# Performance work log

Hardware: AMD Instinct MI355X
Metric: run time of the kernel (lower is better)

Reference implementation:

```python
import jax, jax.numpy as jnp
import numpy as np

IN_DIM = 128
D_MODEL = 2 * IN_DIM        # 256, Mamba d_model
D_INNER = 2 * D_MODEL       # 512, expand=2
D_STATE = 16
D_CONV = 4
DT_RANK = (D_MODEL + 15) // 16  # 16
B = 4
C = 1024                    # original channel dim -> Mamba sequence length
EPS = 1e-5


def rmsnorm(x, w):
    return x * jax.lax.rsqrt(jnp.mean(x * x, axis=-1, keepdims=True) + EPS) * w


def conv1x1(x, w, b):
    # x: (B, Cin, L); 1x1 conv == channel matmul
    return jnp.einsum('oi,bil->bol', w, x) + b[None, :, None]


def mamba(u, in_w, conv_w, conv_b, xproj_w, dt_w, dt_b, A_log, Dp, out_w):
    # u: (B, L, D_MODEL) -- faithful mamba_ssm Mamba block (defaults)
    di, K = conv_w.shape
    n = A_log.shape[1]
    r = dt_w.shape[1]
    xz = u @ in_w.T                              # (B,L,2*di)
    xx, z = jnp.split(xz, 2, axis=-1)
    # depthwise causal conv over L
    xt = jnp.pad(jnp.transpose(xx, (0, 2, 1)), ((0, 0), (0, 0), (K - 1, 0)))
    xc = jax.lax.conv_general_dilated(xt, conv_w[:, None, :], (1,), 'VALID',
                                      feature_group_count=di)
    xx = jax.nn.silu(jnp.transpose(xc + conv_b[None, :, None], (0, 2, 1)))
    dbl = xx @ xproj_w.T                         # (B,L,r+2n)
    dt, Bm, Cm = dbl[..., :r], dbl[..., r:r + n], dbl[..., r + n:]
    dt = jax.nn.softplus(dt @ dt_w.T + dt_b)     # (B,L,di)
    A = -jnp.exp(A_log)                          # (di,n)
    dA = jnp.exp(dt[..., None] * A)              # (B,L,di,n)
    dBx = (dt * xx)[..., None] * Bm[:, :, None, :]

    def step(h, inps):
        dA_t, dBx_t, C_t = inps
        h = dA_t * h + dBx_t
        return h, jnp.einsum('bdn,bn->bd', h, C_t)

    h0 = jnp.zeros((u.shape[0], di, n), u.dtype)
    _, ys = jax.lax.scan(step, h0, (jnp.moveaxis(dA, 1, 0),
                                    jnp.moveaxis(dBx, 1, 0),
                                    jnp.moveaxis(Cm, 1, 0)))
    y = jnp.moveaxis(ys, 0, 1) + xx * Dp
    return (y * jax.nn.silu(z)) @ out_w.T


def postnorm_mamba(u, params, norm_w):
    return rmsnorm(mamba(u, *params), norm_w) + u


def _forward(x, W_in, b_in, W_wp, b_wp, W_fp, b_fp, W_bp, b_bp, W_out, b_out,
             norm_w_top,
             f_in_w, f_conv_w, f_conv_b, f_xproj_w, f_dt_w, f_dt_b, f_A_log, f_D, f_out_w, f_norm_w,
             bk_in_w, bk_conv_w, bk_conv_b, bk_xproj_w, bk_dt_w, bk_dt_b, bk_A_log, bk_D, bk_out_w, bk_norm_w):
    residual = x                                  # (B, C, L)
    xn = rmsnorm(x, norm_w_top)                   # RMSNorm over L
    xt = jnp.transpose(xn, (0, 2, 1))             # (B, L, C); L acts as conv channels
    ssm_in = conv1x1(xt, W_in, b_in)              # (B, 2L, C)
    # forward branch
    fwd = conv1x1(ssm_in, W_fp, b_fp)
    fwd = jnp.transpose(fwd, (0, 2, 1))           # (B, C, 2L): Mamba seq=C
    fwd = postnorm_mamba(fwd, (f_in_w, f_conv_w, f_conv_b, f_xproj_w, f_dt_w,
                               f_dt_b, f_A_log, f_D, f_out_w), f_norm_w)
    fwd = jnp.transpose(fwd, (0, 2, 1))           # (B, 2L, C)
    # backward branch (flip along C)
    bwd = conv1x1(ssm_in[:, :, ::-1], W_bp, b_bp)
    bwd = jnp.transpose(bwd, (0, 2, 1))
    bwd = postnorm_mamba(bwd, (bk_in_w, bk_conv_w, bk_conv_b, bk_xproj_w, bk_dt_w,
                               bk_dt_b, bk_A_log, bk_D, bk_out_w), bk_norm_w)
    bwd = jnp.transpose(bwd, (0, 2, 1))[:, :, ::-1]
    # swish gate
    w = conv1x1(xt, W_wp, b_wp)
    w = w * jax.nn.sigmoid(w)
    out = conv1x1(w * fwd + w * bwd, W_out, b_out)  # (B, L, C)
    return jnp.transpose(out, (0, 2, 1)) + residual  # (B, C, L)


def setup_inputs():
    key = jax.random.key(0)
    ks = iter(jax.random.split(key, 64))
    rn = lambda shape, s=0.02: jax.random.normal(next(ks), shape, jnp.float32) * s
    inp = {"x": jax.random.normal(next(ks), (B, C, IN_DIM), jnp.float32)}
    inp["W_in"] = rn((2 * IN_DIM, IN_DIM));   inp["b_in"] = rn((2 * IN_DIM,), 0.1)
    inp["W_wp"] = rn((2 * IN_DIM, IN_DIM));   inp["b_wp"] = rn((2 * IN_DIM,), 0.1)
    inp["W_fp"] = rn((2 * IN_DIM, 2 * IN_DIM)); inp["b_fp"] = rn((2 * IN_DIM,), 0.1)
    inp["W_bp"] = rn((2 * IN_DIM, 2 * IN_DIM)); inp["b_bp"] = rn((2 * IN_DIM,), 0.1)
    inp["W_out"] = rn((IN_DIM, 2 * IN_DIM));  inp["b_out"] = rn((IN_DIM,), 0.1)
    inp["norm_w_top"] = jnp.ones((IN_DIM,), jnp.float32)
    A_init = jnp.log(jnp.broadcast_to(jnp.arange(1, D_STATE + 1, dtype=jnp.float32),
                                      (D_INNER, D_STATE)))
    for p in ("f", "bk"):
        inp[p + "_in_w"] = rn((2 * D_INNER, D_MODEL))
        inp[p + "_conv_w"] = rn((D_INNER, D_CONV), 0.2)
        inp[p + "_conv_b"] = rn((D_INNER,), 0.1)
        inp[p + "_xproj_w"] = rn((DT_RANK + 2 * D_STATE, D_INNER))
        inp[p + "_dt_w"] = rn((D_INNER, DT_RANK), 0.1)
        inp[p + "_dt_b"] = rn((D_INNER,), 0.5)
        inp[p + "_A_log"] = A_init
        inp[p + "_D"] = jnp.ones((D_INNER,), jnp.float32)
        inp[p + "_out_w"] = rn((D_MODEL, D_INNER))
        inp[p + "_norm_w"] = jnp.ones((D_MODEL,), jnp.float32)
    return inp


def reference(x, W_in, b_in, W_wp, b_wp, W_fp, b_fp, W_bp, b_bp, W_out, b_out,
              norm_w_top,
              f_in_w, f_conv_w, f_conv_b, f_xproj_w, f_dt_w, f_dt_b, f_A_log, f_D, f_out_w, f_norm_w,
              bk_in_w, bk_conv_w, bk_conv_b, bk_xproj_w, bk_dt_w, bk_dt_b, bk_A_log, bk_D, bk_out_w, bk_norm_w):
    return _forward(x, W_in, b_in, W_wp, b_wp, W_fp, b_fp, W_bp, b_bp, W_out, b_out,
                    norm_w_top,
                    f_in_w, f_conv_w, f_conv_b, f_xproj_w, f_dt_w, f_dt_b, f_A_log, f_D, f_out_w, f_norm_w,
                    bk_in_w, bk_conv_w, bk_conv_b, bk_xproj_w, bk_dt_w, bk_dt_b, bk_A_log, bk_D, bk_out_w, bk_norm_w)
```

## Files before the change

### kernel.cpp

```cpp
#include <hip/hip_runtime.h>
#include <math.h>

#define C_LEN 1024
#define NROW 4096
#define NCHUNK 32
#define CHUNK 32

typedef __attribute__((ext_vector_type(8))) short short8;
typedef __attribute__((ext_vector_type(4))) float f32x4;

__device__ __forceinline__ float siluf(float x) { return x / (1.f + __expf(-x)); }

__device__ __forceinline__ unsigned short f2bf(float f) {
    unsigned u = __builtin_bit_cast(unsigned, f);
    unsigned r = (u + 0x7FFFu + ((u >> 16) & 1u)) >> 16;
    return (unsigned short)r;
}
__device__ __forceinline__ float bf2f(unsigned short v) {
    unsigned u = ((unsigned)v) << 16;
    return __builtin_bit_cast(float, u);
}

struct WTab {
    const float* s[11];
    unsigned short* d[11];
    int n[11];
};
__global__ __launch_bounds__(256) void k_prep(WTab t, const float* __restrict__ x,
                                              const float* __restrict__ nw,
                                              unsigned short* __restrict__ xn_bf) {
    int seg = blockIdx.y;
    if (seg < 11) {
        int n = t.n[seg];
        int i = (blockIdx.x * 256 + threadIdx.x) * 4;
        if (i < n) {
            float4 v = *(const float4*)(t.s[seg] + i);
            unsigned short* o = t.d[seg] + i;
            o[0] = f2bf(v.x); o[1] = f2bf(v.y); o[2] = f2bf(v.z); o[3] = f2bf(v.w);
        }
    } else {
        int wave = threadIdx.x >> 6, lane = threadIdx.x & 63;
        #pragma unroll
        for (int it = 0; it < 4; ++it) {
            int row = blockIdx.x * 16 + it * 4 + wave;
            float2 v = ((const float2*)(x + (size_t)row * 128))[lane];
            float ss = v.x * v.x + v.y * v.y;
            #pragma unroll
            for (int off = 32; off; off >>= 1) ss += __shfl_xor(ss, off, 64);
            float rs = rsqrtf(ss * (1.f / 128.f) + 1e-5f);
            float2 wv = ((const float2*)nw)[lane];
            ushort2 o;
            o.x = f2bf(v.x * rs * wv.x);
            o.y = f2bf(v.y * rs * wv.y);
            ((ushort2*)(xn_bf + (size_t)row * 128))[lane] = o;
        }
    }
}

__global__ __launch_bounds__(256) void k_gemm_bf(const unsigned short* __restrict__ A,
                                                 const unsigned short* __restrict__ W,
                                                 const float* __restrict__ bias,
                                                 unsigned short* __restrict__ Cbf,
                                                 int N, int K) {
    __shared__ __align__(16) unsigned short As[64 * 72];
    __shared__ __align__(16) unsigned short Bs[64 * 72];
    int tid = threadIdx.x;
    int m0 = blockIdx.y * 64, n0 = blockIdx.x * 64;
    int w = tid >> 6, lane = tid & 63;
    int q = lane >> 4, ln = lane & 15;
    int srow = tid >> 2;
    int sseg = (tid & 3) * 16;

    const unsigned short* pa = A + (size_t)(m0 + srow) * K + sseg;
    const unsigned short* pw = W + (size_t)(n0 + srow) * K + sseg;

    f32x4 acc[4];
    #pragma unroll
    for (int j = 0; j < 4; ++j) acc[j] = (f32x4)(0.f);

    for (int k0 = 0; k0 < K; k0 += 64) {
        *(short8*)&As[srow * 72 + sseg]     = *(const short8*)pa;
        *(short8*)&As[srow * 72 + sseg + 8] = *(const short8*)(pa + 8);
        *(short8*)&Bs[srow * 72 + sseg]     = *(const short8*)pw;
        *(short8*)&Bs[srow * 72 + sseg + 8] = *(const short8*)(pw + 8);
        pa += 64; pw += 64;
        __syncthreads();
        short8 af0 = *(const short8*)&As[(w * 16 + ln) * 72 + q * 8];
        short8 af1 = *(const short8*)&As[(w * 16 + ln) * 72 + 32 + q * 8];
        #pragma unroll
        for (int j = 0; j < 4; ++j) {
            short8 bf0 = *(const short8*)&Bs[(j * 16 + ln) * 72 + q * 8];
            short8 bf1 = *(const short8*)&Bs[(j * 16 + ln) * 72 + 32 + q * 8];
            acc[j] = __builtin_amdgcn_mfma_f32_16x16x32_bf16(af0, bf0, acc[j], 0, 0, 0);
            acc[j] = __builtin_amdgcn_mfma_f32_16x16x32_bf16(af1, bf1, acc[j], 0, 0, 0);
        }
        __syncthreads();
    }
    #pragma unroll
    for (int j = 0; j < 4; ++j) {
        int nn = n0 + j * 16 + ln;
        float bsv = bias[nn];
        #pragma unroll
        for (int r = 0; r < 4; ++r) {
            int m = m0 + w * 16 + q * 4 + r;
            Cbf[(size_t)m * N + nn] = f2bf(acc[j][r] + bsv);
        }
    }
}

__global__ __launch_bounds__(256) void k_gemm3(
        const unsigned short* __restrict__ xn, const unsigned short* __restrict__ ssm,
        const unsigned short* __restrict__ Wfp, const unsigned short* __restrict__ Wbp,
        const unsigned short* __restrict__ Wwp,
        const float* __restrict__ bfp, const float* __restrict__ bbp,
        const float* __restrict__ bwp,
        unsigned short* __restrict__ uf, unsigned short* __restrict__ ub,
        unsigned short* __restrict__ wbuf) {
    __shared__ __align__(16) unsigned short As[64 * 72];
    __shared__ __align__(16) unsigned short Bs[64 * 72];
    int z = blockIdx.z;
    const unsigned short* A = (z == 2) ? xn : ssm;
    const unsigned short* W = (z == 0) ? Wfp : (z == 1) ? Wbp : Wwp;
    const float* bias = (z == 0) ? bfp : (z == 1) ? bbp : bwp;
    unsigned short* C = (z == 0) ? uf : (z == 1) ? ub : wbuf;
    int K = (z == 2) ? 128 : 256;
    int tid = threadIdx.x;
    int m0 = blockIdx.y * 64, n0 = blockIdx.x * 64;
    int w = tid >> 6, lane = tid & 63;
    int q = lane >> 4, ln = lane & 15;
    int srow = tid >> 2;
    int sseg = (tid & 3) * 16;

    int mLog = m0 + srow;
    int mPhys = (z == 1) ? (mLog ^ (C_LEN - 1)) : mLog;
    const unsigned short* pa = A + (size_t)mPhys * K + sseg;
    const unsigned short* pw = W + (size_t)(n0 + srow) * K + sseg;

    f32x4 acc[4];
    #pragma unroll
    for (int j = 0; j < 4; ++j) acc[j] = (f32x4)(0.f);

    for (int k0 = 0; k0 < K; k0 += 64) {
        *(short8*)&As[srow * 72 + sseg]     = *(const short8*)pa;
        *(short8*)&As[srow * 72 + sseg + 8] = *(const short8*)(pa + 8);
        *(short8*)&Bs[srow * 72 + sseg]     = *(const short8*)pw;
        *(short8*)&Bs[srow * 72 + sseg + 8] = *(const short8*)(pw + 8);
        pa += 64; pw += 64;
        __syncthreads();
        short8 af0 = *(const short8*)&As[(w * 16 + ln) * 72 + q * 8];
        short8 af1 = *(const short8*)&As[(w * 16 + ln) * 72 + 32 + q * 8];
        #pragma unroll
        for (int j = 0; j < 4; ++j) {
            short8 bf0 = *(const short8*)&Bs[(j * 16 + ln) * 72 + q * 8];
            short8 bf1 = *(const short8*)&Bs[(j * 16 + ln) * 72 + 32 + q * 8];
            acc[j] = __builtin_amdgcn_mfma_f32_16x16x32_bf16(af0, bf0, acc[j], 0, 0, 0);
            acc[j] = __builtin_amdgcn_mfma_f32_16x16x32_bf16(af1, bf1, acc[j], 0, 0, 0);
        }
        __syncthreads();
    }
    #pragma unroll
    for (int j = 0; j < 4; ++j) {
        int nn = n0 + j * 16 + ln;
        float bsv = bias[nn];
        #pragma unroll
        for (int r = 0; r < 4; ++r) {
            int m = m0 + w * 16 + q * 4 + r;
            float v = acc[j][r] + bsv;
            if (z == 2) v = siluf(v);
            C[(size_t)m * 256 + nn] = f2bf(v);
        }
    }
}

__global__ __launch_bounds__(256) void k_gemm128(
        const unsigned short* __restrict__ A0, const unsigned short* __restrict__ A1,
        const unsigned short* __restrict__ W0, const unsigned short* __restrict__ W1,
        unsigned short* __restrict__ Cb0, unsigned short* __restrict__ Cb1,
        int N, int K) {
    __shared__ __align__(16) unsigned short As[128 * 72];
    __shared__ __align__(16) unsigned short Bs[64 * 72];
    int p = blockIdx.z;
    const unsigned short* A = p ? A1 : A0;
    const unsigned short* W = p ? W1 : W0;
    unsigned short* Cbf = p ? Cb1 : Cb0;
    int tid = threadIdx.x;
    int m0 = blockIdx.y * 128, n0 = blockIdx.x * 64;
    int w = tid >> 6, lane = tid & 63;
    int q = lane >> 4, ln = lane & 15;

    int arow0 = tid >> 1;
    int aseg0 = (tid & 1) * 32;
    int brow = tid >> 2, bseg = (tid & 3) * 16;
    const unsigned short* pa = A + (size_t)(m0 + arow0) * K + aseg0;
    const unsigned short* pw = W + (size_t)(n0 + brow) * K + bseg;

    f32x4 acc[2][4];
    #pragma unroll
    for (int i = 0; i < 2; ++i)
        #pragma unroll
        for (int j = 0; j < 4; ++j) acc[i][j] = (f32x4)(0.f);

    for (int k0 = 0; k0 < K; k0 += 64) {
        #pragma unroll
        for (int h = 0; h < 4; ++h)
            *(short8*)&As[arow0 * 72 + aseg0 + h * 8] = *(const short8*)(pa + h * 8);
        *(short8*)&Bs[brow * 72 + bseg]     = *(const short8*)pw;
        *(short8*)&Bs[brow * 72 + bseg + 8] = *(const short8*)(pw + 8);
        pa += 64; pw += 64;
        __syncthreads();
        short8 a0[2], a1[2];
        #pragma unroll
        for (int i = 0; i < 2; ++i) {
            int row = w * 32 + i * 16 + ln;
            a0[i] = *(const short8*)&As[row * 72 + q * 8];
            a1[i] = *(const short8*)&As[row * 72 + 32 + q * 8];
        }
        #pragma unroll
        for (int j = 0; j < 4; ++j) {
            short8 bf0 = *(const short8*)&Bs[(j * 16 + ln) * 72 + q * 8];
            short8 bf1 = *(const short8*)&Bs[(j * 16 + ln) * 72 + 32 + q * 8];
            #pragma unroll
            for (int i = 0; i < 2; ++i) {
                acc[i][j] = __builtin_amdgcn_mfma_f32_16x16x32_bf16(a0[i], bf0, acc[i][j], 0, 0, 0);
                acc[i][j] = __builtin_amdgcn_mfma_f32_16x16x32_bf16(a1[i], bf1, acc[i][j], 0, 0, 0);
            }
        }
        __syncthreads();
    }
    #pragma unroll
    for (int i = 0; i < 2; ++i)
        #pragma unroll
        for (int j = 0; j < 4; ++j) {
            int nn = n0 + j * 16 + ln;
            #pragma unroll
            for (int r = 0; r < 4; ++r) {
                int m = m0 + w * 32 + i * 16 + q * 4 + r;
                Cbf[(size_t)m * N + nn] = f2bf(acc[i][j][r]);
            }
        }
}

__global__ __launch_bounds__(256) void k_gemm2f(
        const unsigned short* __restrict__ A0, const unsigned short* __restrict__ A1,
        const unsigned short* __restrict__ W0, const unsigned short* __restrict__ W1,
        float* __restrict__ Cf0, float* __restrict__ Cf1,
        int N, int K) {
    __shared__ __align__(16) unsigned short As[64 * 72];
    __shared__ __align__(16) unsigned short Bs[64 * 72];
    int p = blockIdx.z;
    const unsigned short* A = p ? A1 : A0;
    const unsigned short* W = p ? W1 : W0;
    float* Cf = p ? Cf1 : Cf0;
    int tid = threadIdx.x;
    int m0 = blockIdx.y * 64, n0 = blockIdx.x * 64;
    int w = tid >> 6, lane = tid & 63;
    int q = lane >> 4, ln = lane & 15;
    int srow = tid >> 2;
    int sseg = (tid & 3) * 16;

    const unsigned short* pa = A + (size_t)(m0 + srow) * K + sseg;
    int nIdx = n0 + srow;
    const unsigned short* pw = W + (size_t)nIdx * K + sseg;
    bool nOK = (nIdx < N);

    f32x4 acc[4];
    #pragma unroll
    for (int j = 0; j < 4; ++j) acc[j] = (f32x4)(0.f);

    for (int k0 = 0; k0 < K; k0 += 64) {
        *(short8*)&As[srow * 72 + sseg]     = *(const short8*)pa;
        *(short8*)&As[srow * 72 + sseg + 8] = *(const short8*)(pa + 8);
        short8 b0 = (short8)(0), b1 = (short8)(0);
        if (nOK) { b0 = *(const short8*)pw; b1 = *(const short8*)(pw + 8); }
        *(short8*)&Bs[srow * 72 + sseg] = b0;
        *(short8*)&Bs[srow * 72 + sseg + 8] = b1;
        pa += 64; pw += 64;
        __syncthreads();
        short8 af0 = *(const short8*)&As[(w * 16 + ln) * 72 + q * 8];
        short8 af1 = *(const short8*)&As[(w * 16 + ln) * 72 + 32 + q * 8];
        #pragma unroll
        for (int j = 0; j < 4; ++j) {
            short8 bf0 = *(const short8*)&Bs[(j * 16 + ln) * 72 + q * 8];
            short8 bf1 = *(const short8*)&Bs[(j * 16 + ln) * 72 + 32 + q * 8];
            acc[j] = __builtin_amdgcn_mfma_f32_16x16x32_bf16(af0, bf0, acc[j], 0, 0, 0);
            acc[j] = __builtin_amdgcn_mfma_f32_16x16x32_bf16(af1, bf1, acc[j], 0, 0, 0);
        }
        __syncthreads();
    }
    #pragma unroll
    for (int j = 0; j < 4; ++j) {
        int nn = n0 + j * 16 + ln;
        if (nn < N) {
            #pragma unroll
            for (int r = 0; r < 4; ++r) {
                int m = m0 + w * 16 + q * 4 + r;
                Cf[(size_t)m * N + nn] = acc[j][r];
            }
        }
    }
}

__global__ __launch_bounds__(256) void k_gemm_comb(const unsigned short* __restrict__ wbuf,
                                                   const unsigned short* __restrict__ mof,
                                                   const unsigned short* __restrict__ mob,
                                                   const unsigned short* __restrict__ W,
                                                   const float* __restrict__ bias,
                                                   const float* __restrict__ resid,
                                                   float* __restrict__ Cf,
                                                   int N, int K) {
    __shared__ __align__(16) unsigned short As[64 * 72];
    __shared__ __align__(16) unsigned short Bs[64 * 72];
    int tid = threadIdx.x;
    int m0 = blockIdx.y * 64, n0 = blockIdx.x * 64;
    int w = tid >> 6, lane = tid & 63;
    int q = lane >> 4, ln = lane & 15;
    int srow = tid >> 2;
    int sseg = (tid & 3) * 16;

    int mLog = m0 + srow;
    int mFlip = mLog ^ (C_LEN - 1);
    int nIdx = n0 + srow;
    const unsigned short* pw = W + (size_t)nIdx * K + sseg;
    bool nOK = (nIdx < N);

    f32x4 acc[4];
    #pragma unroll
    for (int j = 0; j < 4; ++j) acc[j] = (f32x4)(0.f);

    for (int k0 = 0; k0 < K; k0 += 64) {
        size_t off  = (size_t)mLog * 256 + k0 + sseg;
        size_t offb = (size_t)mFlip * 256 + k0 + sseg;
        #pragma unroll
        for (int h = 0; h < 2; ++h) {
            short8 aw = *(const short8*)(wbuf + off + h * 8);
            short8 af = *(const short8*)(mof + off + h * 8);
            short8 ab = *(const short8*)(mob + offb + h * 8);
            short8 av;
            #pragma unroll
            for (int j = 0; j < 8; ++j)
                av[j] = (short)f2bf(bf2f((unsigned short)aw[j]) *
                                    (bf2f((unsigned short)af[j]) + bf2f((unsigned short)ab[j])));
            *(short8*)&As[srow * 72 + sseg + h * 8] = av;
        }
        short8 b0 = (short8)(0), b1 = (short8)(0);
        if (nOK) { b0 = *(const short8*)pw; b1 = *(const short8*)(pw + 8); }
        *(short8*)&Bs[srow * 72 + sseg] = b0;
        *(short8*)&Bs[srow * 72 + sseg + 8] = b1;
        pw += 64;
        __syncthreads();
        short8 af0 = *(const short8*)&As[(w * 16 + ln) * 72 + q * 8];
        short8 af1 = *(const short8*)&As[(w * 16 + ln) * 72 + 32 + q * 8];
        #pragma unroll
        for (int j = 0; j < 4; ++j) {
            short8 bf0 = *(const short8*)&Bs[(j * 16 + ln) * 72 + q * 8];
            short8 bf1 = *(const short8*)&Bs[(j * 16 + ln) * 72 + 32 + q * 8];
            acc[j] = __builtin_amdgcn_mfma_f32_16x16x32_bf16(af0, bf0, acc[j], 0, 0, 0);
            acc[j] = __builtin_amdgcn_mfma_f32_16x16x32_bf16(af1, bf1, acc[j], 0, 0, 0);
        }
        __syncthreads();
    }
    #pragma unroll
    for (int j = 0; j < 4; ++j) {
        int nn = n0 + j * 16 + ln;
        if (nn < N) {
            float bsv = bias[nn];
            #pragma unroll
            for (int r = 0; r < 4; ++r) {
                int m = m0 + w * 16 + q * 4 + r;
                Cf[(size_t)m * N + nn] = acc[j][r] + bsv + resid[(size_t)m * N + nn];
            }
        }
    }
}

__global__ __launch_bounds__(256) void k_conv(const unsigned short* __restrict__ xz0,
                                              const unsigned short* __restrict__ xz1,
                                              const float* __restrict__ cw0,
                                              const float* __restrict__ cw1,
                                              const float* __restrict__ cb0,
                                              const float* __restrict__ cb1,
                                              unsigned short* __restrict__ xc0,
                                              unsigned short* __restrict__ xc1) {
    int pz = blockIdx.z;
    const unsigned short* xz = pz ? xz1 : xz0;
    const float* cw = pz ? cw1 : cw0;
    const float* cb = pz ? cb1 : cb0;
    unsigned short* xconv_bf = pz ? xc1 : xc0;
    int d = blockIdx.x * 256 + threadIdx.x;
    int by = blockIdx.y;
    int b = by >> 6, c0 = (by & 63) * 16;
    float4 cwv = *(const float4*)(cw + d * 4);
    float bias = cb[d];
    const unsigned short* base = xz + (size_t)(b * C_LEN) * 1024 + d;
    float w0 = 0.f, w1 = 0.f, w2 = 0.f;
    if (c0) {
        w0 = bf2f(base[(size_t)(c0 - 3) * 1024]);
        w1 = bf2f(base[(size_t)(c0 - 2) * 1024]);
        w2 = bf2f(base[(size_t)(c0 - 1) * 1024]);
    }
    unsigned short* out = xconv_bf + (size_t)(b * C_LEN + c0) * 512 + d;
    #pragma unroll
    for (int i = 0; i < 16; ++i) {
        float cur = bf2f(base[(size_t)(c0 + i) * 1024]);
        float acc = bias;
        acc = fmaf(cwv.x, w0, acc);
        acc = fmaf(cwv.y, w1, acc);
        acc = fmaf(cwv.z, w2, acc);
        acc = fmaf(cwv.w, cur, acc);
        out[(size_t)i * 512] = f2bf(siluf(acc));
        w0 = w1; w1 = w2; w2 = cur;
    }
}

__global__ __launch_bounds__(256) void k_dtproj(const float* __restrict__ dbl0,
                                                const float* __restrict__ dbl1,
                                                const float* __restrict__ dtw0,
                                                const float* __restrict__ dtw1,
                                                const float* __restrict__ dtb0,
                                                const float* __restrict__ dtb1,
                                                unsigned short* __restrict__ dt0,
                                                unsigned short* __restrict__ dt1) {
    int pz = blockIdx.z;
    const float* dbl = pz ? dbl1 : dbl0;
    const float* dtw = pz ? dtw1 : dtw0;
    const float* dtb = pz ? dtb1 : dtb0;
    unsigned short* dt = pz ? dt1 : dt0;
    int d = blockIdx.x * 256 + threadIdx.x;
    int r0 = blockIdx.y * 8;
    float4 w0 = *(const float4*)(dtw + d * 16);
    float4 w1 = *(const float4*)(dtw + d * 16 + 4);
    float4 w2 = *(const float4*)(dtw + d * 16 + 8);
    float4 w3 = *(const float4*)(dtw + d * 16 + 12);
    float bias = dtb[d];
    #pragma unroll
    for (int rr = 0; rr < 8; ++rr) {
        int r = r0 + rr;
        const float* row = dbl + (size_t)r * 48;
        float s = bias;
        s = fmaf(row[0], w0.x, s);  s = fmaf(row[1], w0.y, s);
        s = fmaf(row[2], w0.z, s);  s = fmaf(row[3], w0.w, s);
        s = fmaf(row[4], w1.x, s);  s = fmaf(row[5], w1.y, s);
        s = fmaf(row[6], w1.z, s);  s = fmaf(row[7], w1.w, s);
        s = fmaf(row[8], w2.x, s);  s = fmaf(row[9], w2.y, s);
        s = fmaf(row[10], w2.z, s); s = fmaf(row[11], w2.w, s);
        s = fmaf(row[12], w3.x, s); s = fmaf(row[13], w3.y, s);
        s = fmaf(row[14], w3.z, s); s = fmaf(row[15], w3.w, s);
        float sp = fmaxf(s, 0.f) + log1pf(__expf(-fabsf(s)));
        dt[(size_t)r * 512 + d] = f2bf(sp);
    }
}

__global__ __launch_bounds__(256) void k_scan1(const unsigned short* __restrict__ dt0,
                                               const unsigned short* __restrict__ dt1,
// ... 67 lines not shown
    #pragma unroll
    for (int k = 0; k < NCHUNK; ++k) {
        size_t idx = (size_t)(b * NCHUNK + k) * 8192 + dn;
        float pv = Pfin[idx];
        float hf = hfin[idx];
        Pfin[idx] = carry;
        carry = fmaf(pv, carry, hf);
    }
}

__global__ __launch_bounds__(256) void k_scan3(const unsigned short* __restrict__ dt0,
                                               const unsigned short* __restrict__ dt1,
                                               const unsigned short* __restrict__ xc0,
                                               const unsigned short* __restrict__ xc1,
                                               const float* __restrict__ dblA,
                                               const float* __restrict__ dblB,
                                               const unsigned short* __restrict__ xz0,
                                               const unsigned short* __restrict__ xz1,
                                               const float* __restrict__ alog0,
                                               const float* __restrict__ alog1,
                                               const float* __restrict__ Dp0,
                                               const float* __restrict__ Dp1,
                                               const float* __restrict__ carry0,
                                               const float* __restrict__ carry1,
                                               unsigned short* __restrict__ g0,
                                               unsigned short* __restrict__ g1) {
    int z = blockIdx.z;
    int b = z & 3, p = z >> 2;
    const unsigned short* dt = p ? dt1 : dt0;
    const unsigned short* xconv_bf = p ? xc1 : xc0;
    const float* dbl = p ? dblB : dblA;
    const unsigned short* xz = p ? xz1 : xz0;
    const float* A_log = p ? alog1 : alog0;
    const float* Dp = p ? Dp1 : Dp0;
    const float* carryArr = p ? carry1 : carry0;
    unsigned short* gated_bf = p ? g1 : g0;
    int tid = threadIdx.x;
    int nh = tid & 1, dl = tid >> 1;
    int k = blockIdx.x, dg = blockIdx.y;
    int d = dg * 128 + dl;
    float4 al0 = *(const float4*)&A_log[d * 16 + nh * 8];
    float4 al1 = *(const float4*)&A_log[d * 16 + nh * 8 + 4];
    float Ac[8] = {-__expf(al0.x), -__expf(al0.y), -__expf(al0.z), -__expf(al0.w),
                   -__expf(al1.x), -__expf(al1.y), -__expf(al1.z), -__expf(al1.w)};
    float Dd = Dp[d];
    size_t idx = ((size_t)(b * NCHUNK + k) * 512 + d) * 16 + nh * 8;
    float4 h0 = *(const float4*)&carryArr[idx];
    float4 h1 = *(const float4*)&carryArr[idx + 4];
    float h[8] = {h0.x, h0.y, h0.z, h0.w, h1.x, h1.y, h1.z, h1.w};
    size_t r0 = (size_t)(b * C_LEN + k * CHUNK);
    const unsigned short* pdt = dt + r0 * 512 + d;
    const unsigned short* pxv = xconv_bf + r0 * 512 + d;
    const float* pB  = dbl + r0 * 48 + 16 + nh * 8;
    const float* pC  = dbl + r0 * 48 + 32 + nh * 8;
    const unsigned short* pz = xz + r0 * 1024 + 512 + d;
    unsigned short* pg = gated_bf + r0 * 512 + d;
    #pragma unroll 4
    for (int c = 0; c < CHUNK; ++c) {
        float dtv = bf2f(*pdt);
        float xv  = bf2f(*pxv);
        float4 B0 = *(const float4*)pB;
        float4 B1 = *(const float4*)(pB + 4);
        float4 C0 = *(const float4*)pC;
        float4 C1 = *(const float4*)(pC + 4);
        float dx = dtv * xv;
        float Bv[8] = {B0.x, B0.y, B0.z, B0.w, B1.x, B1.y, B1.z, B1.w};
        float Cv[8] = {C0.x, C0.y, C0.z, C0.w, C1.x, C1.y, C1.z, C1.w};
        float contrib = 0.f;
        #pragma unroll
        for (int j = 0; j < 8; ++j) {
            h[j] = fmaf(__expf(dtv * Ac[j]), h[j], dx * Bv[j]);
            contrib = fmaf(h[j], Cv[j], contrib);
        }
        contrib += __shfl_xor(contrib, 1, 64);
        if (nh == 0) {
            float y = contrib + xv * Dd;
            float zv = bf2f(*pz);
            *pg = f2bf(y * siluf(zv));
        }
        pdt += 512; pxv += 512; pB += 48; pC += 48; pz += 1024; pg += 512;
    }
}

__global__ __launch_bounds__(256) void k_postnorm(const unsigned short* __restrict__ mo0,
                                                  const unsigned short* __restrict__ mo1,
                                                  const float* __restrict__ w0,
                                                  const float* __restrict__ w1,
                                                  const unsigned short* __restrict__ u0,
                                                  const unsigned short* __restrict__ u1,
                                                  unsigned short* __restrict__ o0,
                                                  unsigned short* __restrict__ o1) {
    __shared__ float red[4];
    int p = blockIdx.y;
    const unsigned short* mo = p ? mo1 : mo0;
    const float* w = p ? w1 : w0;
    const unsigned short* u = p ? u1 : u0;
    unsigned short* out = p ? o1 : o0;
    int r = blockIdx.x, tid = threadIdx.x;
    float v = bf2f(mo[(size_t)r * 256 + tid]);
    float ss = v * v;
    #pragma unroll
    for (int off = 32; off; off >>= 1) ss += __shfl_xor(ss, off, 64);
    if ((tid & 63) == 0) red[tid >> 6] = ss;
    __syncthreads();
    float tot = red[0] + red[1] + red[2] + red[3];
    float rs = rsqrtf(tot * (1.f / 256.f) + 1e-5f);
    out[(size_t)r * 256 + tid] = f2bf(v * rs * w[tid] + bf2f(u[(size_t)r * 256 + tid]));
}

extern "C" void kernel_launch(void* const* d_in, const int* in_sizes, int n_in,
                              void* d_out, int out_size, void* d_ws, size_t ws_size,
                              hipStream_t stream) {
    const float* x          = (const float*)d_in[0];
    const float* W_in       = (const float*)d_in[1];
    const float* b_in       = (const float*)d_in[2];
    const float* W_wp       = (const float*)d_in[3];
    const float* b_wp       = (const float*)d_in[4];
    const float* W_fp       = (const float*)d_in[5];
    const float* b_fp       = (const float*)d_in[6];
    const float* W_bp       = (const float*)d_in[7];
    const float* b_bp       = (const float*)d_in[8];
    const float* W_out      = (const float*)d_in[9];
    const float* b_out      = (const float*)d_in[10];
    const float* norm_w_top = (const float*)d_in[11];
    const float* mamba_p[2][10];
    for (int p = 0; p < 2; ++p)
        for (int i = 0; i < 10; ++i)
            mamba_p[p][i] = (const float*)d_in[12 + p * 10 + i];

    float* ws = (float*)d_ws;
    float* dblP[2]  = {ws + 0,       ws + 196608};
    float* hfinP[2] = {ws + 4587520, ws + 5636096};
    float* PfinP[2] = {ws + 6684672, ws + 7733248};
    unsigned short* dtsP[2] = {(unsigned short*)(ws + 393216),
                               (unsigned short*)(ws + 2490368)};

    unsigned short* us = (unsigned short*)(ws + 8781824);
    unsigned short* xn_bf   = us + 0;
    unsigned short* ssm_bf  = us + 524288;
    unsigned short* uf_bf   = us + 1572864;
    unsigned short* ub_bf   = us + 2621440;
    unsigned short* wbuf_bf = us + 3670016;
    unsigned short* xzP[2]  = {us + 4718592,  us + 8912896};
    unsigned short* xcP[2]  = {us + 13107200, us + 15204352};
    unsigned short* gP[2]   = {us + 17301504, us + 19398656};
    unsigned short* moP[2]  = {us + 21495808, us + 22544384};
    unsigned short* mof_bf  = us + 23592960;
    unsigned short* mob_bf  = us + 24641536;
    unsigned short* wb      = us + 25690112;
    unsigned short* wb_W_in  = wb + 0;
    unsigned short* wb_W_wp  = wb + 32768;
    unsigned short* wb_W_fp  = wb + 65536;
    unsigned short* wb_W_bp  = wb + 131072;
    unsigned short* wb_W_out = wb + 196608;
    unsigned short* wb_in[2]  = {wb + 229376, wb + 647168};
    unsigned short* wb_xp[2]  = {wb + 491520, wb + 909312};
    unsigned short* wb_outw[2]= {wb + 516096, wb + 933888};

    WTab t;
    t.s[0] = W_in;            t.d[0] = wb_W_in;   t.n[0] = 32768;
    t.s[1] = W_wp;            t.d[1] = wb_W_wp;   t.n[1] = 32768;
    t.s[2] = W_fp;            t.d[2] = wb_W_fp;   t.n[2] = 65536;
    t.s[3] = W_bp;            t.d[3] = wb_W_bp;   t.n[3] = 65536;
    t.s[4] = W_out;           t.d[4] = wb_W_out;  t.n[4] = 32768;
    t.s[5] = mamba_p[0][0];   t.d[5] = wb_in[0];  t.n[5] = 262144;
    t.s[6] = mamba_p[0][3];   t.d[6] = wb_xp[0];  t.n[6] = 24576;
    t.s[7] = mamba_p[0][8];   t.d[7] = wb_outw[0];t.n[7] = 131072;
    t.s[8] = mamba_p[1][0];   t.d[8] = wb_in[1];  t.n[8] = 262144;
    t.s[9] = mamba_p[1][3];   t.d[9] = wb_xp[1];  t.n[9] = 24576;
    t.s[10]= mamba_p[1][8];   t.d[10]= wb_outw[1];t.n[10]= 131072;
    k_prep<<<dim3(256, 12), 256, 0, stream>>>(t, x, norm_w_top, xn_bf);

    k_gemm_bf<<<dim3(4, 64), 256, 0, stream>>>(xn_bf, wb_W_in, b_in, ssm_bf, 256, 128);
    k_gemm3<<<dim3(4, 64, 3), 256, 0, stream>>>(xn_bf, ssm_bf, wb_W_fp, wb_W_bp, wb_W_wp,
                                                b_fp, b_bp, b_wp, uf_bf, ub_bf, wbuf_bf);
    k_gemm128<<<dim3(16, 32, 2), 256, 0, stream>>>(uf_bf, ub_bf, wb_in[0], wb_in[1],
                                                   xzP[0], xzP[1], 1024, 256);
    k_conv<<<dim3(2, 256, 2), 256, 0, stream>>>(xzP[0], xzP[1],
                                                mamba_p[0][1], mamba_p[1][1],
                                                mamba_p[0][2], mamba_p[1][2],
                                                xcP[0], xcP[1]);
    k_gemm2f<<<dim3(1, 64, 2), 256, 0, stream>>>(xcP[0], xcP[1], wb_xp[0], wb_xp[1],
                                                 dblP[0], dblP[1], 48, 512);
    k_dtproj<<<dim3(2, 512, 2), 256, 0, stream>>>(dblP[0], dblP[1],
                                                  mamba_p[0][4], mamba_p[1][4],
                                                  mamba_p[0][5], mamba_p[1][5],
                                                  dtsP[0], dtsP[1]);
    k_scan1<<<dim3(NCHUNK, 4, 8), 256, 0, stream>>>(dtsP[0], dtsP[1], xcP[0], xcP[1],
                                                    dblP[0], dblP[1],
                                                    mamba_p[0][6], mamba_p[1][6],
                                                    hfinP[0], hfinP[1], PfinP[0], PfinP[1]);
    k_scan2<<<256, 256, 0, stream>>>(hfinP[0], hfinP[1], PfinP[0], PfinP[1]);
    k_scan3<<<dim3(NCHUNK, 4, 8), 256, 0, stream>>>(dtsP[0], dtsP[1], xcP[0], xcP[1],
                                                    dblP[0], dblP[1], xzP[0], xzP[1],
                                                    mamba_p[0][6], mamba_p[1][6],
                                                    mamba_p[0][7], mamba_p[1][7],
                                                    PfinP[0], PfinP[1], gP[0], gP[1]);
    k_gemm128<<<dim3(4, 32, 2), 256, 0, stream>>>(gP[0], gP[1], wb_outw[0], wb_outw[1],
                                                  moP[0], moP[1], 256, 512);
    k_postnorm<<<dim3(NROW, 2), 256, 0, stream>>>(moP[0], moP[1],
                                                  mamba_p[0][9], mamba_p[1][9],
                                                  uf_bf, ub_bf, mof_bf, mob_bf);
    k_gemm_comb<<<dim3(2, 64), 256, 0, stream>>>(wbuf_bf, mof_bf, mob_bf, wb_W_out, b_out,
                                                 x, (float*)d_out, 128, 256);
}
```

Measured before the change: 254.2 us.

## Fold chained linear projections into one combined weight matrix and a single mega-GEMM

Because the input projection, the forward/backward projections and each Mamba in_proj are all linear, their products are precomputed per call (W_fp·W_in, then in_w·(W_fp·W_in), plus the matching biases). All of these become slices of one stacked weight, so a single 128-row-tile GEMM over the normalized input produces uf, ub, wbuf and both xz tensors, and the flip is applied in the epilogue. This removes the chained GEMMs and the intermediate activations between them. The postnorm and the gate-combine are also fused into one kernel that writes the combined A operand, which simplifies the final GEMM. In exchange, two small fp32 weight-combination kernels with naive dot loops are added, and rounding changes because the weights are combined in fp32 and then cast to bf16.

```diff
diff --git a/kernel.cpp b/kernel.cpp
--- a/kernel.cpp
+++ b/kernel.cpp
@@ -22,15 +22,25 @@
 }
 
 struct WTab {
-    const float* s[11];
-    unsigned short* d[11];
-    int n[11];
+    const float* s[6];
+    unsigned short* d[6];
+    int n[6];
 };
 __global__ __launch_bounds__(256) void k_prep(WTab t, const float* __restrict__ x,
                                               const float* __restrict__ nw,
-                                              unsigned short* __restrict__ xn_bf) {
+                                              unsigned short* __restrict__ xn_bf,
+                                              const float* __restrict__ W_fp,
+                                              const float* __restrict__ W_bp,
+                                              const float* __restrict__ W_in,
+                                              const float* __restrict__ b_in,
+                                              const float* __restrict__ b_fp,
+                                              const float* __restrict__ b_bp,
+                                              const float* __restrict__ b_wp,
+                                              float* __restrict__ Wpin,
+                                              float* __restrict__ bmega,
+                                              unsigned short* __restrict__ Wmega) {
     int seg = blockIdx.y;
-    if (seg < 11) {
+    if (seg < 6) {
         int n = t.n[seg];
         int i = (blockIdx.x * 256 + threadIdx.x) * 4;
         if (i < n) {
@@ -38,136 +48,154 @@
             unsigned short* o = t.d[seg] + i;
             o[0] = f2bf(v.x); o[1] = f2bf(v.y); o[2] = f2bf(v.z); o[3] = f2bf(v.w);
         }
-    } else {
+    } else if (seg == 6) {
         int wave = threadIdx.x >> 6, lane = threadIdx.x & 63;
         #pragma unroll
         for (int it = 0; it < 4; ++it) {
             int row = blockIdx.x * 16 + it * 4 + wave;
-            float2 v = ((const float2*)(x + (size_t)row * 128))[lane];
-            float ss = v.x * v.x + v.y * v.y;
-            #pragma unroll
-            for (int off = 32; off; off >>= 1) ss += __shfl_xor(ss, off, 64);
-            float rs = rsqrtf(ss * (1.f / 128.f) + 1e-5f);
-            float2 wv = ((const float2*)nw)[lane];
-            ushort2 o;
-            o.x = f2bf(v.x * rs * wv.x);
-            o.y = f2bf(v.y * rs * wv.y);
-            ((ushort2*)(xn_bf + (size_t)row * 128))[lane] = o;
-        }
-    }
-}
-
-__global__ __launch_bounds__(256) void k_gemm_bf(const unsigned short* __restrict__ A,
-                                                 const unsigned short* __restrict__ W,
-                                                 const float* __restrict__ bias,
-                                                 unsigned short* __restrict__ Cbf,
-                                                 int N, int K) {
-    __shared__ __align__(16) unsigned short As[64 * 72];
+            if (row < 4096) {
+                float2 v = ((const float2*)(x + (size_t)row * 128))[lane];
+                float ss = v.x * v.x + v.y * v.y;
+                #pragma unroll
+                for (int off = 32; off; off >>= 1) ss += __shfl_xor(ss, off, 64);
+                float rs = rsqrtf(ss * (1.f / 128.f) + 1e-5f);
+                float2 wv = ((const float2*)nw)[lane];
+                ushort2 o;
+                o.x = f2bf(v.x * rs * wv.x);
+                o.y = f2bf(v.y * rs * wv.y);
+                ((ushort2*)(xn_bf + (size_t)row * 128))[lane] = o;
+            }
+        }
+    } else {
+        int tg = blockIdx.x * 256 + threadIdx.x;
+        if (tg < 65536) {
+            int p = tg >> 15, rem = tg & 32767;
+            int o = rem >> 7, i = rem & 127;
+            const float* Wsrc = p ? W_bp : W_fp;
+            float s = 0.f;
+            #pragma unroll 8
+            for (int j = 0; j < 256; ++j) s += Wsrc[o * 256 + j] * W_in[j * 128 + i];
+            Wpin[p * 32768 + o * 128 + i] = s;
+            Wmega[(size_t)(p * 256 + o) * 128 + i] = f2bf(s);
+        } else if (tg < 66048) {
+            int q = tg - 65536;
+            int p = q >> 8, o = q & 255;
+            const float* Wsrc = p ? W_bp : W_fp;
+            const float* badd = p ? b_bp : b_fp;
+            float s = badd[o];
+            #pragma unroll 8
+            for (int j = 0; j < 256; ++j) s += Wsrc[o * 256 + j] * b_in[j];
+            bmega[p * 256 + o] = s;
+        } else if (tg < 66304) {
+            int q = tg - 66048;
+            bmega[512 + q] = b_wp[q];
+        }
+    }
+}
+
+__global__ __launch_bounds__(256) void k_wcomb2(const float* __restrict__ f_in_w,
+                                                const float* __restrict__ bk_in_w,
+                                                const float* __restrict__ Wpin,
+                                                unsigned short* __restrict__ Wmega,
+                                                float* __restrict__ bmega) {
+    int tg = blockIdx.x * 256 + threadIdx.x;
+    if (tg < 262144) {
+        int p = tg >> 17, rem = tg & 131071;
+        int o = rem >> 7, i = rem & 127;
+        const float* inw = p ? bk_in_w : f_in_w;
+        const float* wp = Wpin + p * 32768;
+        float s = 0.f;
+        #pragma unroll 8
+        for (int j = 0; j < 256; ++j) s += inw[o * 256 + j] * wp[j * 128 + i];
+        Wmega[(size_t)(768 + p * 1024 + o) * 128 + i] = f2bf(s);
+    } else if (tg < 264192) {
+        int q = tg - 262144;
+        int p = q >> 10, o = q & 1023;
+        const float* inw = p ? bk_in_w : f_in_w;
+        const float* bp = bmega + p * 256;
+        float s = 0.f;
+        #pragma unroll 8
+        for (int j = 0; j < 256; ++j) s += inw[o * 256 + j] * bp[j];
+        bmega[768 + p * 1024 + o] = s;
+    }
+}
+
+__global__ __launch_bounds__(256) void k_megagemm(const unsigned short* __restrict__ A,
+                                                  const unsigned short* __restrict__ W,
+                                                  const float* __restrict__ bias,
+                                                  unsigned short* __restrict__ uf,
+                                                  unsigned short* __restrict__ ub,
+                                                  unsigned short* __restrict__ wbuf,
+                                                  unsigned short* __restrict__ xzF,
+                                                  unsigned short* __restrict__ xzB) {
+    __shared__ __align__(16) unsigned short As[128 * 72];
     __shared__ __align__(16) unsigned short Bs[64 * 72];
+    const int K = 128;
     int tid = threadIdx.x;
-    int m0 = blockIdx.y * 64, n0 = blockIdx.x * 64;
+    int m0 = blockIdx.y * 128, n0 = blockIdx.x * 64;
     int w = tid >> 6, lane = tid & 63;
     int q = lane >> 4, ln = lane & 15;
-    int srow = tid >> 2;
-    int sseg = (tid & 3) * 16;
-
-    const unsigned short* pa = A + (size_t)(m0 + srow) * K + sseg;
-    const unsigned short* pw = W + (size_t)(n0 + srow) * K + sseg;
-
-    f32x4 acc[4];
-    #pragma unroll
-    for (int j = 0; j < 4; ++j) acc[j] = (f32x4)(0.f);
+
+    unsigned short* Cb; int stride, nc0; bool flip = false, dosilu = false;
+    if (n0 < 256)       { Cb = uf;   stride = 256;  nc0 = n0; }
+    else if (n0 < 512)  { Cb = ub;   stride = 256;  nc0 = n0 - 256;  flip = true; }
+    else if (n0 < 768)  { Cb = wbuf; stride = 256;  nc0 = n0 - 512;  dosilu = true; }
+    else if (n0 < 1792) { Cb = xzF;  stride = 1024; nc0 = n0 - 768; }
+    else                { Cb = xzB;  stride = 1024; nc0 = n0 - 1792; flip = true; }
+
+    int arow0 = tid >> 1;
+    int aseg0 = (tid & 1) * 32;
+    int brow = tid >> 2, bseg = (tid & 3) * 16;
+    const unsigned short* pa = A + (size_t)(m0 + arow0) * K + aseg0;
+    const unsigned short* pw = W + (size_t)(n0 + brow) * K + bseg;
+
+    f32x4 acc[2][4];
+    #pragma unroll
+    for (int i = 0; i < 2; ++i)
+        #pragma unroll
+        for (int j = 0; j < 4; ++j) acc[i][j] = (f32x4)(0.f);
 
     for (int k0 = 0; k0 < K; k0 += 64) {
-        *(short8*)&As[srow * 72 + sseg]     = *(const short8*)pa;
-        *(short8*)&As[srow * 72 + sseg + 8] = *(const short8*)(pa + 8);
-        *(short8*)&Bs[srow * 72 + sseg]     = *(const short8*)pw;
-        *(short8*)&Bs[srow * 72 + sseg + 8] = *(const short8*)(pw + 8);
+        #pragma unroll
+        for (int h = 0; h < 4; ++h)
+            *(short8*)&As[arow0 * 72 + aseg0 + h * 8] = *(const short8*)(pa + h * 8);
+        *(short8*)&Bs[brow * 72 + bseg]     = *(const short8*)pw;
+        *(short8*)&Bs[brow * 72 + bseg + 8] = *(const short8*)(pw + 8);
         pa += 64; pw += 64;
         __syncthreads();
-        short8 af0 = *(const short8*)&As[(w * 16 + ln) * 72 + q * 8];
-        short8 af1 = *(const short8*)&As[(w * 16 + ln) * 72 + 32 + q * 8];
+        short8 a0[2], a1[2];
+        #pragma unroll
+        for (int i = 0; i < 2; ++i) {
+            int row = w * 32 + i * 16 + ln;
+            a0[i] = *(const short8*)&As[row * 72 + q * 8];
+            a1[i] = *(const short8*)&As[row * 72 + 32 + q * 8];
+        }
         #pragma unroll
         for (int j = 0; j < 4; ++j) {
             short8 bf0 = *(const short8*)&Bs[(j * 16 + ln) * 72 + q * 8];
             short8 bf1 = *(const short8*)&Bs[(j * 16 + ln) * 72 + 32 + q * 8];
-            acc[j] = __builtin_amdgcn_mfma_f32_16x16x32_bf16(af0, bf0, acc[j], 0, 0, 0);
-            acc[j] = __builtin_amdgcn_mfma_f32_16x16x32_bf16(af1, bf1, acc[j], 0, 0, 0);
+            #pragma unroll
+            for (int i = 0; i < 2; ++i) {
+                acc[i][j] = __builtin_amdgcn_mfma_f32_16x16x32_bf16(a0[i], bf0, acc[i][j], 0, 0, 0);
+                acc[i][j] = __builtin_amdgcn_mfma_f32_16x16x32_bf16(a1[i], bf1, acc[i][j], 0, 0, 0);
+            }
         }
         __syncthreads();
     }
     #pragma unroll
     for (int j = 0; j < 4; ++j) {
-        int nn = n0 + j * 16 + ln;
-        float bsv = bias[nn];
-        #pragma unroll
-        for (int r = 0; r < 4; ++r) {
-            int m = m0 + w * 16 + q * 4 + r;
-            Cbf[(size_t)m * N + nn] = f2bf(acc[j][r] + bsv);
-        }
-    }
-}
-
-__global__ __launch_bounds__(256) void k_gemm3(
-        const unsigned short* __restrict__ xn, const unsigned short* __restrict__ ssm,
-        const unsigned short* __restrict__ Wfp, const unsigned short* __restrict__ Wbp,
-        const unsigned short* __restrict__ Wwp,
-        const float* __restrict__ bfp, const float* __restrict__ bbp,
-        const float* __restrict__ bwp,
-        unsigned short* __restrict__ uf, unsigned short* __restrict__ ub,
-        unsigned short* __restrict__ wbuf) {
-    __shared__ __align__(16) unsigned short As[64 * 72];
-    __shared__ __align__(16) unsigned short Bs[64 * 72];
-    int z = blockIdx.z;
-    const unsigned short* A = (z == 2) ? xn : ssm;
-    const unsigned short* W = (z == 0) ? Wfp : (z == 1) ? Wbp : Wwp;
-    const float* bias = (z == 0) ? bfp : (z == 1) ? bbp : bwp;
-    unsigned short* C = (z == 0) ? uf : (z == 1) ? ub : wbuf;
-    int K = (z == 2) ? 128 : 256;
-    int tid = threadIdx.x;
-    int m0 = blockIdx.y * 64, n0 = blockIdx.x * 64;
-    int w = tid >> 6, lane = tid & 63;
-    int q = lane >> 4, ln = lane & 15;
-    int srow = tid >> 2;
-    int sseg = (tid & 3) * 16;
-
-    int mLog = m0 + srow;
-    int mPhys = (z == 1) ? (mLog ^ (C_LEN - 1)) : mLog;
-    const unsigned short* pa = A + (size_t)mPhys * K + sseg;
-    const unsigned short* pw = W + (size_t)(n0 + srow) * K + sseg;
-
-    f32x4 acc[4];
-    #pragma unroll
-    for (int j = 0; j < 4; ++j) acc[j] = (f32x4)(0.f);
-
-    for (int k0 = 0; k0 < K; k0 += 64) {
-        *(short8*)&As[srow * 72 + sseg]     = *(const short8*)pa;
-        *(short8*)&As[srow * 72 + sseg + 8] = *(const short8*)(pa + 8);
-        *(short8*)&Bs[srow * 72 + sseg]     = *(const short8*)pw;
-        *(short8*)&Bs[srow * 72 + sseg + 8] = *(const short8*)(pw + 8);
-        pa += 64; pw += 64;
-        __syncthreads();
-        short8 af0 = *(const short8*)&As[(w * 16 + ln) * 72 + q * 8];
-        short8 af1 = *(const short8*)&As[(w * 16 + ln) * 72 + 32 + q * 8];
-        #pragma unroll
-        for (int j = 0; j < 4; ++j) {
-            short8 bf0 = *(const short8*)&Bs[(j * 16 + ln) * 72 + q * 8];
-            short8 bf1 = *(const short8*)&Bs[(j * 16 + ln) * 72 + 32 + q * 8];
-            acc[j] = __builtin_amdgcn_mfma_f32_16x16x32_bf16(af0, bf0, acc[j], 0, 0, 0);
-            acc[j] = __builtin_amdgcn_mfma_f32_16x16x32_bf16(af1, bf1, acc[j], 0, 0, 0);
-        }
-        __syncthreads();
-    }
-    #pragma unroll
-    for (int j = 0; j < 4; ++j) {
-        int nn = n0 + j * 16 + ln;
-        float bsv = bias[nn];
-        #pragma unroll
-        for (int r = 0; r < 4; ++r) {
-            int m = m0 + w * 16 + q * 4 + r;
-            float v = acc[j][r] + bsv;
-            if (z == 2) v = siluf(v);
-            C[(size_t)m * 256 + nn] = f2bf(v);
+        float bsv = bias[n0 + j * 16 + ln];
+        int nc = nc0 + j * 16 + ln;
+        #pragma unroll
+        for (int i = 0; i < 2; ++i) {
+            #pragma unroll
+            for (int r = 0; r < 4; ++r) {
+                int m = m0 + w * 32 + i * 16 + q * 4 + r;
+                int mw = flip ? (m ^ (C_LEN - 1)) : m;
+                float v = acc[i][j][r] + bsv;
+                if (dosilu) v = siluf(v);
+                Cb[(size_t)mw * stride + nc] = f2bf(v);
+            }
         }
     }
 }
@@ -300,16 +328,14 @@
     }
 }
 
-__global__ __launch_bounds__(256) void k_gemm_comb(const unsigned short* __restrict__ wbuf,
-                                                   const unsigned short* __restrict__ mof,
-                                                   const unsigned short* __restrict__ mob,
-                                                   const unsigned short* __restrict__ W,
-                                                   const float* __restrict__ bias,
-                                                   const float* __restrict__ resid,
-                                                   float* __restrict__ Cf,
-                                                   int N, int K) {
+__global__ __launch_bounds__(256) void k_gemm_out(const unsigned short* __restrict__ A,
+                                                  const unsigned short* __restrict__ W,
+                                                  const float* __restrict__ bias,
+                                                  const float* __restrict__ resid,
+                                                  float* __restrict__ Cf) {
     __shared__ __align__(16) unsigned short As[64 * 72];
     __shared__ __align__(16) unsigned short Bs[64 * 72];
+    const int N = 128, K = 256;
     int tid = threadIdx.x;
     int m0 = blockIdx.y * 64, n0 = blockIdx.x * 64;
     int w = tid >> 6, lane = tid & 63;
@@ -317,36 +343,19 @@
     int srow = tid >> 2;
     int sseg = (tid & 3) * 16;
 
-    int mLog = m0 + srow;
-    int mFlip = mLog ^ (C_LEN - 1);
-    int nIdx = n0 + srow;
-    const unsigned short* pw = W + (size_t)nIdx * K + sseg;
-    bool nOK = (nIdx < N);
+    const unsigned short* pa = A + (size_t)(m0 + srow) * K + sseg;
+    const unsigned short* pw = W + (size_t)(n0 + srow) * K + sseg;
 
     f32x4 acc[4];
     #pragma unroll
     for (int j = 0; j < 4; ++j) acc[j] = (f32x4)(0.f);
 
     for (int k0 = 0; k0 < K; k0 += 64) {
-        size_t off  = (size_t)mLog * 256 + k0 + sseg;
-        size_t offb = (size_t)mFlip * 256 + k0 + sseg;
-        #pragma unroll
-        for (int h = 0; h < 2; ++h) {
-            short8 aw = *(const short8*)(wbuf + off + h * 8);
-            short8 af = *(const short8*)(mof + off + h * 8);
-            short8 ab = *(const short8*)(mob + offb + h * 8);
-            short8 av;
-            #pragma unroll
-            for (int j = 0; j < 8; ++j)
-                av[j] = (short)f2bf(bf2f((unsigned short)aw[j]) *
-                                    (bf2f((unsigned short)af[j]) + bf2f((unsigned short)ab[j])));
-            *(short8*)&As[srow * 72 + sseg + h * 8] = av;
-        }
-        short8 b0 = (short8)(0), b1 = (short8)(0);
-        if (nOK) { b0 = *(const short8*)pw; b1 = *(const short8*)(pw + 8); }
-        *(short8*)&Bs[srow * 72 + sseg] = b0;
-        *(short8*)&Bs[srow * 72 + sseg + 8] = b1;
-        pw += 64;
+        *(short8*)&As[srow * 72 + sseg]     = *(const short8*)pa;
+        *(short8*)&As[srow * 72 + sseg + 8] = *(const short8*)(pa + 8);
+        *(short8*)&Bs[srow * 72 + sseg]     = *(const short8*)pw;
+        *(short8*)&Bs[srow * 72 + sseg + 8] = *(const short8*)(pw + 8);
+        pa += 64; pw += 64;
         __syncthreads();
         short8 af0 = *(const short8*)&As[(w * 16 + ln) * 72 + q * 8];
         short8 af1 = *(const short8*)&As[(w * 16 + ln) * 72 + 32 + q * 8];
@@ -362,13 +371,11 @@
     #pragma unroll
     for (int j = 0; j < 4; ++j) {
         int nn = n0 + j * 16 + ln;
-        if (nn < N) {
-            float bsv = bias[nn];
-            #pragma unroll
-            for (int r = 0; r < 4; ++r) {
-                int m = m0 + w * 16 + q * 4 + r;
-                Cf[(size_t)m * N + nn] = acc[j][r] + bsv + resid[(size_t)m * N + nn];
-            }
+        float bsv = bias[nn];
+        #pragma unroll
+        for (int r = 0; r < 4; ++r) {
+            int m = m0 + w * 16 + q * 4 + r;
+            Cf[(size_t)m * N + nn] = acc[j][r] + bsv + resid[(size_t)m * N + nn];
         }
     }
 }
@@ -602,30 +609,32 @@
     }
 }
 
-__global__ __launch_bounds__(256) void k_postnorm(const unsigned short* __restrict__ mo0,
+__global__ __launch_bounds__(256) void k_postcomb(const unsigned short* __restrict__ mo0,
                                                   const unsigned short* __restrict__ mo1,
                                                   const float* __restrict__ w0,
                                                   const float* __restrict__ w1,
-                                                  const unsigned short* __restrict__ u0,
-                                                  const unsigned short* __restrict__ u1,
-                                                  unsigned short* __restrict__ o0,
-                                                  unsigned short* __restrict__ o1) {
-    __shared__ float red[4];
-    int p = blockIdx.y;
-    const unsigned short* mo = p ? mo1 : mo0;
-    const float* w = p ? w1 : w0;
-    const unsigned short* u = p ? u1 : u0;
-    unsigned short* out = p ? o1 : o0;
-    int r = blockIdx.x, tid = threadIdx.x;
-    float v = bf2f(mo[(size_t)r * 256 + tid]);
-    float ss = v * v;
-    #pragma unroll
-    for (int off = 32; off; off >>= 1) ss += __shfl_xor(ss, off, 64);
-    if ((tid & 63) == 0) red[tid >> 6] = ss;
+                                                  const unsigned short* __restrict__ uf,
+                                                  const unsigned short* __restrict__ ub,
+                                                  const unsigned short* __restrict__ wbuf,
+                                                  unsigned short* __restrict__ Acomb) {
+    __shared__ float red[8];
+    int r = blockIdx.x, t = threadIdx.x;
+    int rf = r ^ (C_LEN - 1);
+    float v0 = bf2f(mo0[(size_t)r * 256 + t]);
+    float v1 = bf2f(mo1[(size_t)rf * 256 + t]);
+    float ss0 = v0 * v0, ss1 = v1 * v1;
+    #pragma unroll
+    for (int off = 32; off; off >>= 1) {
+        ss0 += __shfl_xor(ss0, off, 64);
+        ss1 += __shfl_xor(ss1, off, 64);
+    }
+    if ((t & 63) == 0) { red[t >> 6] = ss0; red[4 + (t >> 6)] = ss1; }
     __syncthreads();
-    float tot = red[0] + red[1] + red[2] + red[3];
-    float rs = rsqrtf(tot * (1.f / 256.f) + 1e-5f);
-    out[(size_t)r * 256 + tid] = f2bf(v * rs * w[tid] + bf2f(u[(size_t)r * 256 + tid]));
+    float rs0 = rsqrtf((red[0] + red[1] + red[2] + red[3]) * (1.f / 256.f) + 1e-5f);
+    float rs1 = rsqrtf((red[4] + red[5] + red[6] + red[7]) * (1.f / 256.f) + 1e-5f);
+    float mofv = v0 * rs0 * w0[t] + bf2f(uf[(size_t)r * 256 + t]);
+    float mobv = v1 * rs1 * w1[t] + bf2f(ub[(size_t)rf * 256 + t]);
+    Acomb[(size_t)r * 256 + t] = f2bf(bf2f(wbuf[(size_t)r * 256 + t]) * (mofv + mobv));
 }
 
 extern "C" void kernel_launch(void* const* d_in, const int* in_sizes, int n_in,
@@ -650,14 +659,16 @@
 
     float* ws = (float*)d_ws;
     float* dblP[2]  = {ws + 0,       ws + 196608};
+    unsigned short* dtsP[2] = {(unsigned short*)(ws + 393216),
+                               (unsigned short*)(ws + 2490368)};
+    float* Wpin  = ws + 1441792;
+    float* bmega = ws + 1507328;
     float* hfinP[2] = {ws + 4587520, ws + 5636096};
     float* PfinP[2] = {ws + 6684672, ws + 7733248};
-    unsigned short* dtsP[2] = {(unsigned short*)(ws + 393216),
-                               (unsigned short*)(ws + 2490368)};
 
     unsigned short* us = (unsigned short*)(ws + 8781824);
     unsigned short* xn_bf   = us + 0;
-    unsigned short* ssm_bf  = us + 524288;
+    unsigned short* Acomb   = us + 524288;
     unsigned short* uf_bf   = us + 1572864;
     unsigned short* ub_bf   = us + 2621440;
     unsigned short* wbuf_bf = us + 3670016;
@@ -665,37 +676,25 @@
     unsigned short* xcP[2]  = {us + 13107200, us + 15204352};
     unsigned short* gP[2]   = {us + 17301504, us + 19398656};
     unsigned short* moP[2]  = {us + 21495808, us + 22544384};
-    unsigned short* mof_bf  = us + 23592960;
-    unsigned short* mob_bf  = us + 24641536;
+    unsigned short* Wmega   = us + 23592960;
     unsigned short* wb      = us + 25690112;
-    unsigned short* wb_W_in  = wb + 0;
-    unsigned short* wb_W_wp  = wb + 32768;
-    unsigned short* wb_W_fp  = wb + 65536;
-    unsigned short* wb_W_bp  = wb + 131072;
     unsigned short* wb_W_out = wb + 196608;
-    unsigned short* wb_in[2]  = {wb + 229376, wb + 647168};
     unsigned short* wb_xp[2]  = {wb + 491520, wb + 909312};
     unsigned short* wb_outw[2]= {wb + 516096, wb + 933888};
 
     WTab t;
-    t.s[0] = W_in;            t.d[0] = wb_W_in;   t.n[0] = 32768;
-    t.s[1] = W_wp;            t.d[1] = wb_W_wp;   t.n[1] = 32768;
-    t.s[2] = W_fp;            t.d[2] = wb_W_fp;   t.n[2] = 65536;
-    t.s[3] = W_bp;            t.d[3] = wb_W_bp;   t.n[3] = 65536;
-    t.s[4] = W_out;           t.d[4] = wb_W_out;  t.n[4] = 32768;
-    t.s[5] = mamba_p[0][0];   t.d[5] = wb_in[0];  t.n[5] = 262144;
-    t.s[6] = mamba_p[0][3];   t.d[6] = wb_xp[0];  t.n[6] = 24576;
-    t.s[7] = mamba_p[0][8];   t.d[7] = wb_outw[0];t.n[7] = 131072;
-    t.s[8] = mamba_p[1][0];   t.d[8] = wb_in[1];  t.n[8] = 262144;
-    t.s[9] = mamba_p[1][3];   t.d[9] = wb_xp[1];  t.n[9] = 24576;
-    t.s[10]= mamba_p[1][8];   t.d[10]= wb_outw[1];t.n[10]= 131072;
-    k_prep<<<dim3(256, 12), 256, 0, stream>>>(t, x, norm_w_top, xn_bf);
-
-    k_gemm_bf<<<dim3(4, 64), 256, 0, stream>>>(xn_bf, wb_W_in, b_in, ssm_bf, 256, 128);
-    k_gemm3<<<dim3(4, 64, 3), 256, 0, stream>>>(xn_bf, ssm_bf, wb_W_fp, wb_W_bp, wb_W_wp,
-                                                b_fp, b_bp, b_wp, uf_bf, ub_bf, wbuf_bf);
-    k_gemm128<<<dim3(16, 32, 2), 256, 0, stream>>>(uf_bf, ub_bf, wb_in[0], wb_in[1],
-                                                   xzP[0], xzP[1], 1024, 256);
+    t.s[0] = W_wp;            t.d[0] = Wmega + 512 * 128; t.n[0] = 32768;
+    t.s[1] = W_out;           t.d[1] = wb_W_out;          t.n[1] = 32768;
+    t.s[2] = mamba_p[0][3];   t.d[2] = wb_xp[0];          t.n[2] = 24576;
+    t.s[3] = mamba_p[0][8];   t.d[3] = wb_outw[0];        t.n[3] = 131072;
+    t.s[4] = mamba_p[1][3];   t.d[4] = wb_xp[1];          t.n[4] = 24576;
+    t.s[5] = mamba_p[1][8];   t.d[5] = wb_outw[1];        t.n[5] = 131072;
+    k_prep<<<dim3(260, 8), 256, 0, stream>>>(t, x, norm_w_top, xn_bf,
+                                             W_fp, W_bp, W_in, b_in, b_fp, b_bp, b_wp,
+                                             Wpin, bmega, Wmega);
+    k_wcomb2<<<1040, 256, 0, stream>>>(mamba_p[0][0], mamba_p[1][0], Wpin, Wmega, bmega);
+    k_megagemm<<<dim3(44, 32), 256, 0, stream>>>(xn_bf, Wmega, bmega,
+                                                 uf_bf, ub_bf, wbuf_bf, xzP[0], xzP[1]);
     k_conv<<<dim3(2, 256, 2), 256, 0, stream>>>(xzP[0], xzP[1],
                                                 mamba_p[0][1], mamba_p[1][1],
                                                 mamba_p[0][2], mamba_p[1][2],
@@ -718,9 +717,8 @@
                                                     PfinP[0], PfinP[1], gP[0], gP[1]);
     k_gemm128<<<dim3(4, 32, 2), 256, 0, stream>>>(gP[0], gP[1], wb_outw[0], wb_outw[1],
                                                   moP[0], moP[1], 256, 512);
-    k_postnorm<<<dim3(NROW, 2), 256, 0, stream>>>(moP[0], moP[1],
-                                                  mamba_p[0][9], mamba_p[1][9],
-                                                  uf_bf, ub_bf, mof_bf, mob_bf);
-    k_gemm_comb<<<dim3(2, 64), 256, 0, stream>>>(wbuf_bf, mof_bf, mob_bf, wb_W_out, b_out,
-                                                 x, (float*)d_out, 128, 256);
-}
+    k_postcomb<<<NROW, 256, 0, stream>>>(moP[0], moP[1],
+                                         mamba_p[0][9], mamba_p[1][9],
+                                         uf_bf, ub_bf, wbuf_bf, Acomb);
+    k_gemm_out<<<dim3(2, 64), 256, 0, stream>>>(Acomb, wb_W_out, b_out, x, (float*)d_out);
+}
```

Measured after the change: 278.3 us. 1.09x slower.
